# Optimization experiments

Hardware: AMD Instinct MI355X
Metric: run time of the kernel (lower is better)

The kernel has to match this reference:

```python
import jax, jax.numpy as jnp
import numpy as np

DIM = 256
NUM_EXPERTS = 16
EXPERT_HIDDEN = 128
ROUTER_HIDDEN = 64
N_TOKENS = 32768


def setup_inputs() -> dict:
    key = jax.random.key(0)
    ks = jax.random.split(key, 9)
    s = lambda fan_in: 1.0 / np.sqrt(fan_in)
    x = jax.random.normal(ks[0], (N_TOKENS, DIM), dtype=jnp.float32)
    # Router params (Linear(DIM,64) -> ReLU -> Linear(64,E))
    r_w1 = jax.random.uniform(ks[1], (DIM, ROUTER_HIDDEN), jnp.float32, -s(DIM), s(DIM))
    r_b1 = jax.random.uniform(ks[2], (ROUTER_HIDDEN,), jnp.float32, -s(DIM), s(DIM))
    r_w2 = jax.random.uniform(ks[3], (ROUTER_HIDDEN, NUM_EXPERTS), jnp.float32, -s(ROUTER_HIDDEN), s(ROUTER_HIDDEN))
    r_b2 = jax.random.uniform(ks[4], (NUM_EXPERTS,), jnp.float32, -s(ROUTER_HIDDEN), s(ROUTER_HIDDEN))
    # Expert params, stacked over experts: Linear(DIM,128) -> Tanh -> Linear(128,DIM)
    e_w1 = jax.random.uniform(ks[5], (NUM_EXPERTS, DIM, EXPERT_HIDDEN), jnp.float32, -s(DIM), s(DIM))
    e_b1 = jax.random.uniform(ks[6], (NUM_EXPERTS, EXPERT_HIDDEN), jnp.float32, -s(DIM), s(DIM))
    e_w2 = jax.random.uniform(ks[7], (NUM_EXPERTS, EXPERT_HIDDEN, DIM), jnp.float32, -s(EXPERT_HIDDEN), s(EXPERT_HIDDEN))
    e_b2 = jax.random.uniform(ks[8], (NUM_EXPERTS, DIM), jnp.float32, -s(EXPERT_HIDDEN), s(EXPERT_HIDDEN))
    return {"x": x, "r_w1": r_w1, "r_b1": r_b1, "r_w2": r_w2, "r_b2": r_b2,
            "e_w1": e_w1, "e_b1": e_b1, "e_w2": e_w2, "e_b2": e_b2}


def reference(x, r_w1, r_b1, r_w2, r_b2, e_w1, e_b1, e_w2, e_b2):
    # Router: softmax(Linear(ReLU(Linear(x)))), temp=1.0
    h_r = jax.nn.relu(x @ r_w1 + r_b1)                      # [N, 64]
    w = jax.nn.softmax(h_r @ r_w2 + r_b2, axis=-1)          # [N, E]
    # All experts densely (faithful to the reference loop), batched over E.
    h = jnp.tanh(jnp.einsum('nd,edh->neh', x, e_w1) + e_b1[None, :, :])   # [N, E, H]
    outs = jnp.einsum('neh,ehd->ned', h, e_w2) + e_b2[None, :, :]         # [N, E, D]
    # Top-2 gating: mask, renormalize, combine.
    top_val, top_idx = jax.lax.top_k(w, 2)                  # [N, 2]
    n = w.shape[0]
    mask = jnp.zeros_like(w).at[jnp.arange(n)[:, None], top_idx].set(1.0)
    w_top = w * mask
    w_top = w_top / (jnp.sum(w_top, axis=-1, keepdims=True) + 1e-8)
    y_pred = jnp.einsum('ne,ned->nd', w_top, outs)          # [N, D]
    return (y_pred, w)
```

## Files before the change

kernel.cpp:

```cpp
#include <hip/hip_runtime.h>
#include <math.h>

#define NT 32768
#define DIM 256
#define NE 16
#define EH 128
#define RH 64
#define TB 128

#define IB (NT * DIM)
#define WS_COUNTS (IB)
#define WS_OFFSETS (IB + 16)
#define WS_CURSORS (IB + 33)
#define WS_NBLK (IB + 49)
#define WS_TABLE (IB + 64)
#define WS_TOKE (IB + 4096)
#define WS_LIST (WS_TOKE + 2 * NT)
#define WS_TOKG (WS_LIST + 2 * NT)
#define WS_LIST_G (WS_TOKG + 2 * NT)
#define WS_END_I (WS_LIST_G + 2 * NT)
#define U_W1T (2 * WS_END_I)
#define U_W2T (U_W1T + NE * DIM * EH)

typedef __attribute__((ext_vector_type(4))) float f32x4;
typedef __attribute__((ext_vector_type(8))) short bf16x8;
typedef __attribute__((ext_vector_type(8))) unsigned short us8;

#define SWZ(b) ((b) ^ (((b) >> 4) & 0x70))

__device__ inline unsigned short f2bf(float f) {
    unsigned int bits = __builtin_bit_cast(unsigned int, f);
    bits += 0x7fffu + ((bits >> 16) & 1u);
    return (unsigned short)(bits >> 16);
}

__global__ __launch_bounds__(256) void router_kernel(
    const float* __restrict__ x,
    const float* __restrict__ rw1, const float* __restrict__ rb1,
    const float* __restrict__ rw2, const float* __restrict__ rb2,
    float* __restrict__ w_out, int* __restrict__ wsi, float* __restrict__ wsf)
{
    __shared__ float xT[64][68];
    __shared__ float w1s[64][64];
    __shared__ float hs[64][68];
    __shared__ float ls[64][20];
    __shared__ int scnt[16];

    const int tid = threadIdx.x;
    const int tok0 = blockIdx.x * 64;
    if (tid < 16) scnt[tid] = 0;

    float acc[4][4];
#pragma unroll
    for (int i = 0; i < 4; ++i)
#pragma unroll
        for (int j = 0; j < 4; ++j) acc[i][j] = 0.f;

    const int tt = (tid & 15) * 4;
    const int hh = (tid >> 4) * 4;

    for (int kc = 0; kc < 4; ++kc) {
        __syncthreads();
#pragma unroll
        for (int i = 0; i < 4; ++i) {
            int idx = tid + 256 * i;
            int t = idx >> 4;
            int d4 = (idx & 15) * 4;
            float4 v = *(const float4*)(x + (size_t)(tok0 + t) * DIM + kc * 64 + d4);
            xT[d4 + 0][t] = v.x; xT[d4 + 1][t] = v.y;
            xT[d4 + 2][t] = v.z; xT[d4 + 3][t] = v.w;
        }
#pragma unroll
        for (int i = 0; i < 4; ++i) {
            int idx = tid + 256 * i;
            int d = idx >> 4;
            int h4 = (idx & 15) * 4;
            *(float4*)&w1s[d][h4] = *(const float4*)(rw1 + (size_t)(kc * 64 + d) * RH + h4);
        }
        __syncthreads();
#pragma unroll 8
        for (int d = 0; d < 64; ++d) {
            const float4 xa4 = *(const float4*)&xT[d][tt];
            const float4 wv4 = *(const float4*)&w1s[d][hh];
            const float xa[4] = {xa4.x, xa4.y, xa4.z, xa4.w};
            const float wv[4] = {wv4.x, wv4.y, wv4.z, wv4.w};
#pragma unroll
            for (int i = 0; i < 4; ++i)
#pragma unroll
                for (int j = 0; j < 4; ++j)
                    acc[i][j] = fmaf(xa[i], wv[j], acc[i][j]);
        }
    }
    __syncthreads();
    {
        const float4 b4 = *(const float4*)(rb1 + hh);
        const float b[4] = {b4.x, b4.y, b4.z, b4.w};
#pragma unroll
        for (int i = 0; i < 4; ++i) {
            float4 hv;
            hv.x = fmaxf(acc[i][0] + b[0], 0.f);
            hv.y = fmaxf(acc[i][1] + b[1], 0.f);
            hv.z = fmaxf(acc[i][2] + b[2], 0.f);
            hv.w = fmaxf(acc[i][3] + b[3], 0.f);
            *(float4*)&hs[tt + i][hh] = hv;
        }
    }
    __syncthreads();
    {
        int tok = tid >> 2;
        int e0 = (tid & 3) * 4;
        float l[4] = {0.f, 0.f, 0.f, 0.f};
#pragma unroll 8
        for (int k = 0; k < 64; ++k) {
            float hv = hs[tok][k];
            float4 wv = *(const float4*)(rw2 + k * NE + e0);
            l[0] = fmaf(hv, wv.x, l[0]);
            l[1] = fmaf(hv, wv.y, l[1]);
            l[2] = fmaf(hv, wv.z, l[2]);
            l[3] = fmaf(hv, wv.w, l[3]);
        }
        float4 lb = *(const float4*)(rb2 + e0);
        ls[tok][e0 + 0] = l[0] + lb.x;
        ls[tok][e0 + 1] = l[1] + lb.y;
        ls[tok][e0 + 2] = l[2] + lb.z;
        ls[tok][e0 + 3] = l[3] + lb.w;
    }
    __syncthreads();
    if (tid < 64) {
        const int tok = tid;
        const int gt = tok0 + tok;
        float v[16];
        float m = -1e30f;
#pragma unroll
        for (int e = 0; e < 16; ++e) { v[e] = ls[tok][e]; m = fmaxf(m, v[e]); }
        float s = 0.f;
#pragma unroll
        for (int e = 0; e < 16; ++e) { v[e] = expf(v[e] - m); s += v[e]; }
        const float inv = 1.0f / s;
#pragma unroll
        for (int e = 0; e < 16; ++e) v[e] *= inv;
#pragma unroll
        for (int e = 0; e < 16; e += 4) {
            float4 wv = make_float4(v[e], v[e + 1], v[e + 2], v[e + 3]);
            *(float4*)(w_out + (size_t)gt * NE + e) = wv;
        }
        float v1 = -1.f, v2 = -1.f; int i1 = 0, i2 = 0;
#pragma unroll
        for (int e = 0; e < 16; ++e) {
            if (v[e] > v1) { v2 = v1; i2 = i1; v1 = v[e]; i1 = e; }
            else if (v[e] > v2) { v2 = v[e]; i2 = e; }
        }
        const float den = v1 + v2 + 1e-8f;
        atomicAdd(&scnt[i1], 1);
        atomicAdd(&scnt[i2], 1);
        wsi[WS_TOKE + 2 * gt + 0] = i1;
        wsi[WS_TOKE + 2 * gt + 1] = i2;
        wsf[WS_TOKG + 2 * gt + 0] = v1 / den;
        wsf[WS_TOKG + 2 * gt + 1] = v2 / den;
    }
    __syncthreads();
    if (tid < 16 && scnt[tid]) atomicAdd(&wsi[WS_COUNTS + tid], scnt[tid]);
}

__global__ __launch_bounds__(256) void wprep_kernel(
    const float* __restrict__ ew1, const float* __restrict__ ew2,
    unsigned short* __restrict__ w1t, unsigned short* __restrict__ w2t)
{
    __shared__ float t[64][65];
    int b = blockIdx.x;
    const float* src; unsigned short* dst; int R, C, tr, tc;
    if (b < 128) {
        int e = b >> 3, t8 = b & 7; tr = t8 >> 1; tc = t8 & 1;
        src = ew1 + (size_t)e * DIM * EH; R = DIM; C = EH;
        dst = w1t + (size_t)e * DIM * EH;
    } else {
        int b2 = b - 128; int e = b2 >> 3, t8 = b2 & 7; tr = t8 & 1; tc = t8 >> 1;
        src = ew2 + (size_t)e * EH * DIM; R = EH; C = DIM;
        dst = w2t + (size_t)e * EH * DIM;
    }
    const int R0 = tr * 64, C0 = tc * 64;
    const int tid = threadIdx.x;
#pragma unroll
    for (int q = 0; q < 4; ++q) {
        int r = (tid >> 4) + q * 16, c = (tid & 15) * 4;
        float4 v = *(const float4*)(src + (size_t)(R0 + r) * C + C0 + c);
        t[r][c] = v.x; t[r][c + 1] = v.y; t[r][c + 2] = v.z; t[r][c + 3] = v.w;
    }
    __syncthreads();
#pragma unroll
    for (int q = 0; q < 2; ++q) {
        int rp = (tid >> 3) + q * 32, c0 = (tid & 7) * 8;
        us8 u;
#pragma unroll
        for (int k = 0; k < 8; ++k) u[k] = f2bf(t[c0 + k][rp]);
        *(us8*)(dst + (size_t)(C0 + rp) * R + R0 + c0) = u;
    }
}

__global__ __launch_bounds__(64) void scan_kernel(int* __restrict__ wsi)
{
    __shared__ int soff[17], snc[16];
    const int tid = threadIdx.x;
    if (tid == 0) {
        int off = 0, nb = 0;
        soff[0] = 0;
        for (int e = 0; e < NE; ++e) {
            int c = wsi[WS_COUNTS + e];
            wsi[WS_CURSORS + e] = off;
            wsi[WS_OFFSETS + e] = off;
            off += c;
            soff[e + 1] = off;
            snc[e] = nb;
            nb += (c + TB - 1) / TB;
        }
        wsi[WS_OFFSETS + NE] = off;
        wsi[WS_NBLK] = nb;
    }
    __syncthreads();
    for (int e = 0; e < NE; ++e) {
        int nc = (soff[e + 1] - soff[e] + TB - 1) / TB;
        for (int k = tid; k < nc; k += 64)
            wsi[WS_TABLE + snc[e] + k] = (e << 16) | k;
    }
}

__global__ __launch_bounds__(256) void scatter_kernel(int* __restrict__ wsi, float* __restrict__ wsf)
{
    __shared__ int scnt[16], sbase[16];
    const int tid = threadIdx.x;
    const int t = blockIdx.x * 256 + tid;
    if (tid < 16) scnt[tid] = 0;
    __syncthreads();
    const int e0 = wsi[WS_TOKE + 2 * t + 0];
    const int e1 = wsi[WS_TOKE + 2 * t + 1];
    const int l0 = atomicAdd(&scnt[e0], 1);
    const int l1 = atomicAdd(&scnt[e1], 1);
    __syncthreads();
    if (tid < 16) sbase[tid] = scnt[tid] ? atomicAdd(&wsi[WS_CURSORS + tid], scnt[tid]) : 0;
    __syncthreads();
    const int p0 = sbase[e0] + l0;
    const int p1 = sbase[e1] + l1;
    wsi[WS_LIST + p0] = (t << 1);
    wsf[WS_LIST_G + p0] = wsf[WS_TOKG + 2 * t + 0];
    wsi[WS_LIST + p1] = (t << 1) | 1;
    wsf[WS_LIST_G + p1] = wsf[WS_TOKG + 2 * t + 1];
}

__global__ __launch_bounds__(256) void expert_kernel(
    const float* __restrict__ x,
    const float* __restrict__ eb1, const float* __restrict__ eb2,
    const unsigned short* __restrict__ w1t, const unsigned short* __restrict__ w2t,
    const int* __restrict__ wsi, const float* __restrict__ wsf,
    float* __restrict__ y, float* __restrict__ part1)
{
    __shared__ unsigned short smem[32768];
    if ((int)blockIdx.x >= wsi[WS_NBLK]) return;

    const int ent = wsi[WS_TABLE + blockIdx.x];
    const int e = ent >> 16;
    const int c = ent & 0xffff;
    const int start = wsi[WS_OFFSETS + e] + c * TB;
    const int cnt = min(TB, wsi[WS_OFFSETS + e + 1] - start);

    const int tid = threadIdx.x;
    const int lane = tid & 63, w = tid >> 6;
    const int wm = w >> 1, wn = w & 1;
    const int l15 = lane & 15;
    const int lk2 = ((lane >> 4) * 8) * 2;
    const int q4 = (lane >> 4) * 4;

    const int sr = tid >> 1, side = tid & 1;
    const int srow = (sr < cnt) ? (wsi[WS_LIST + start + sr] >> 1) : -1;

    char* lds = (char*)smem;

    f32x4 zero4; zero4[0] = zero4[1] = zero4[2] = zero4[3] = 0.f;
    f32x4 acc[4][4];
#pragma unroll
    for (int i = 0; i < 4; ++i)
#pragma unroll
        for (int j = 0; j < 4; ++j) acc[i][j] = zero4;

    for (int kh = 0; kh < 2; ++kh) {
        __syncthreads();
        {
            const int base = sr * 256 + side * 128;
            const float* xr = x + (size_t)(srow < 0 ? 0 : srow) * DIM + kh * 128 + side * 64;
#pragma unroll
            for (int i = 0; i < 8; ++i) {
                us8 u;
                if (srow >= 0) {
                    float4 a = *(const float4*)(xr + i * 8);
                    float4 b = *(const float4*)(xr + i * 8 + 4);
                    u[0] = f2bf(a.x); u[1] = f2bf(a.y); u[2] = f2bf(a.z); u[3] = f2bf(a.w);
                    u[4] = f2bf(b.x); u[5] = f2bf(b.y); u[6] = f2bf(b.z); u[7] = f2bf(b.w);
                } else {
#pragma unroll
                    for (int k = 0; k < 8; ++k) u[k] = 0;
                }
                *(us8*)(lds + SWZ(base + i * 16)) = u;
            }
        }
        {
            const unsigned short* wr = w1t + (size_t)e * DIM * EH + sr * 256 + kh * 128 + side * 64;
            const int base = 32768 + sr * 256 + side * 128;
#pragma unroll
            for (int i = 0; i < 8; ++i)
                *(us8*)(lds + SWZ(base + i * 16)) = *(const us8*)(wr + i * 8);
        }
        __syncthreads();
#pragma unroll
        for (int ks = 0; ks < 4; ++ks) {
            bf16x8 a[4], b[4];
#pragma unroll
            for (int mt = 0; mt < 4; ++mt) {
                int row = wm * 64 + mt * 16 + l15;
                a[mt] = *(const bf16x8*)(lds + SWZ(row * 256 + ks * 64 + lk2));
            }
#pragma unroll
            for (int nt = 0; nt < 4; ++nt) {
                int h = wn * 64 + nt * 16 + l15;
                b[nt] = *(const bf16x8*)(lds + SWZ(32768 + h * 256 + ks * 64 + lk2));
            }
#pragma unroll
            for (int mt = 0; mt < 4; ++mt)
#pragma unroll
                for (int nt = 0; nt < 4; ++nt)
                    acc[mt][nt] = __builtin_amdgcn_mfma_f32_16x16x32_bf16(a[mt], b[nt], acc[mt][nt], 0, 0, 0);
        }
    }

    __syncthreads();
#pragma unroll
    for (int nt = 0; nt < 4; ++nt) {
        const int col = wn * 64 + nt * 16 + l15;
        const float b1v = eb1[e * EH + col];
#pragma unroll
        for (int mt = 0; mt < 4; ++mt)
#pragma unroll
            for (int r = 0; r < 4; ++r) {
                int row = wm * 64 + mt * 16 + q4 + r;
                *(unsigned short*)(lds + SWZ(row * 256 + col * 2)) = f2bf(tanhf(acc[mt][nt][r] + b1v));
            }
    }
    {
        const unsigned short* wr = w2t + (size_t)e * EH * DIM + (size_t)sr * 128 + side * 64;
        const int base = 32768 + sr * 256 + side * 128;
#pragma unroll
        for (int i = 0; i < 8; ++i)
            *(us8*)(lds + SWZ(base + i * 16)) = *(const us8*)(wr + i * 8);
    }
    __syncthreads();

    for (int dh = 0; dh < 2; ++dh) {
        if (dh == 1) {
            __syncthreads();
            const unsigned short* wr = w2t + (size_t)e * EH * DIM + (size_t)(128 + sr) * 128 + side * 64;
            const int base = 32768 + sr * 256 + side * 128;
#pragma unroll
            for (int i = 0; i < 8; ++i)
                *(us8*)(lds + SWZ(base + i * 16)) = *(const us8*)(wr + i * 8);
            __syncthreads();
        }
        f32x4 acc2[4][4];
#pragma unroll
        for (int i = 0; i < 4; ++i)
#pragma unroll
            for (int j = 0; j < 4; ++j) acc2[i][j] = zero4;
#pragma unroll
        for (int ks = 0; ks < 4; ++ks) {
            bf16x8 a[4], b[4];
#pragma unroll
            for (int mt = 0; mt < 4; ++mt) {
                int row = wm * 64 + mt * 16 + l15;
                a[mt] = *(const bf16x8*)(lds + SWZ(row * 256 + ks * 64 + lk2));
            }
#pragma unroll
            for (int nt = 0; nt < 4; ++nt) {
                int d = wn * 64 + nt * 16 + l15;
                b[nt] = *(const bf16x8*)(lds + SWZ(32768 + d * 256 + ks * 64 + lk2));
            }
#pragma unroll
            for (int mt = 0; mt < 4; ++mt)
#pragma unroll
                for (int nt = 0; nt < 4; ++nt)
                    acc2[mt][nt] = __builtin_amdgcn_mfma_f32_16x16x32_bf16(a[mt], b[nt], acc2[mt][nt], 0, 0, 0);
        }
        float b2v[4];
#pragma unroll
        for (int nt = 0; nt < 4; ++nt)
            b2v[nt] = eb2[e * DIM + dh * 128 + wn * 64 + nt * 16 + l15];
#pragma unroll
        for (int mt = 0; mt < 4; ++mt)
#pragma unroll
            for (int r = 0; r < 4; ++r) {
                int rl = wm * 64 + mt * 16 + q4 + r;
                if (rl < cnt) {
                    int entry = wsi[WS_LIST + start + rl];
                    int tok = entry >> 1;
                    float g = wsf[WS_LIST_G + start + rl];
                    float* dst = ((entry & 1) ? part1 : y) + (size_t)tok * DIM + dh * 128 + wn * 64;
#pragma unroll
                    for (int nt = 0; nt < 4; ++nt)
                        dst[nt * 16 + l15] = g * (acc2[mt][nt][r] + b2v[nt]);
                }
            }
    }
}

__global__ __launch_bounds__(256) void combine_kernel(float* __restrict__ y,
                                                      const float* __restrict__ part1)
{
    const size_t i = ((size_t)blockIdx.x * 256 + threadIdx.x) * 4;
    float4 a = *(float4*)(y + i);
    const float4 b = *(const float4*)(part1 + i);
    a.x += b.x; a.y += b.y; a.z += b.z; a.w += b.w;
    *(float4*)(y + i) = a;
}

extern "C" void kernel_launch(void* const* d_in, const int* in_sizes, int n_in,
                              void* d_out, int out_size, void* d_ws, size_t ws_size,
                              hipStream_t stream)
{
    const float* x = (const float*)d_in[0];
    const float* rw1 = (const float*)d_in[1];
    const float* rb1 = (const float*)d_in[2];
    const float* rw2 = (const float*)d_in[3];
    const float* rb2 = (const float*)d_in[4];
    const float* ew1 = (const float*)d_in[5];
    const float* eb1 = (const float*)d_in[6];
    const float* ew2 = (const float*)d_in[7];
    const float* eb2 = (const float*)d_in[8];

    float* y = (float*)d_out;
    float* w_out = y + (size_t)NT * DIM;
    int* wsi = (int*)d_ws;
    float* wsf = (float*)d_ws;
    float* part1 = (float*)d_ws;
    unsigned short* wsu = (unsigned short*)d_ws;

    hipMemsetAsync(wsi + WS_COUNTS, 0, NE * sizeof(int), stream);

    wprep_kernel<<<256, 256, 0, stream>>>(ew1, ew2, wsu + U_W1T, wsu + U_W2T);
    router_kernel<<<NT / 64, 256, 0, stream>>>(x, rw1, rb1, rw2, rb2, w_out, wsi, wsf);
    scan_kernel<<<1, 64, 0, stream>>>(wsi);
    scatter_kernel<<<NT / 256, 256, 0, stream>>>(wsi, wsf);
    expert_kernel<<<2 * NT / TB + NE, 256, 0, stream>>>(x, eb1, eb2, wsu + U_W1T, wsu + U_W2T,
                                                        wsi, wsf, y, part1);
    combine_kernel<<<NT * DIM / 1024, 256, 0, stream>>>(y, part1);
}
```

Baseline: 129.6 us.

## Shrink expert tile to 64 tokens and read weights straight from global

Halves the token tile per block to 64 rows and stages only the activation tile in LDS (32 KB), with each wave reading its expert weight fragments directly from global/L2 instead of staging them in LDS. The goal is more resident blocks per CU (launch bounds 4), fewer barriers and better load balance across the per-expert chunks. The cost is less weight reuse per block: weights are fetched twice as often overall, and uncoalesced per-lane global reads now feed the MFMAs directly, which can stall them.

```diff
diff --git a/kernel.cpp b/kernel.cpp
--- a/kernel.cpp
+++ b/kernel.cpp
@@ -6,7 +6,7 @@
 #define NE 16
 #define EH 128
 #define RH 64
-#define TB 128
+#define TB 64
 
 #define IB (NT * DIM)
 #define WS_COUNTS (IB)
@@ -26,7 +26,8 @@
 typedef __attribute__((ext_vector_type(8))) short bf16x8;
 typedef __attribute__((ext_vector_type(8))) unsigned short us8;
 
-#define SWZ(b) ((b) ^ (((b) >> 4) & 0x70))
+#define SWZ9(b) ((b) ^ (((b) >> 5) & 0x70))
+#define SWZ8(b) ((b) ^ (((b) >> 4) & 0x70))
 
 __device__ inline unsigned short f2bf(float f) {
     unsigned int bits = __builtin_bit_cast(unsigned int, f);
@@ -246,14 +247,14 @@
     wsf[WS_LIST_G + p1] = wsf[WS_TOKG + 2 * t + 1];
 }
 
-__global__ __launch_bounds__(256) void expert_kernel(
+__global__ __launch_bounds__(256, 4) void expert_kernel(
     const float* __restrict__ x,
     const float* __restrict__ eb1, const float* __restrict__ eb2,
     const unsigned short* __restrict__ w1t, const unsigned short* __restrict__ w2t,
     const int* __restrict__ wsi, const float* __restrict__ wsf,
     float* __restrict__ y, float* __restrict__ part1)
 {
-    __shared__ unsigned short smem[32768];
+    __shared__ unsigned short smem[16384];
     if ((int)blockIdx.x >= wsi[WS_NBLK]) return;
 
     const int ent = wsi[WS_TABLE + blockIdx.x];
@@ -264,144 +265,115 @@
 
     const int tid = threadIdx.x;
     const int lane = tid & 63, w = tid >> 6;
-    const int wm = w >> 1, wn = w & 1;
     const int l15 = lane & 15;
-    const int lk2 = ((lane >> 4) * 8) * 2;
-    const int q4 = (lane >> 4) * 4;
-
-    const int sr = tid >> 1, side = tid & 1;
-    const int srow = (sr < cnt) ? (wsi[WS_LIST + start + sr] >> 1) : -1;
-
+    const int kq = lane >> 4;
+    const int q4 = kq * 4;
     char* lds = (char*)smem;
 
+    {
+        const int row = tid >> 2, q = tid & 3;
+        const int srow = (row < cnt) ? (wsi[WS_LIST + start + row] >> 1) : -1;
+        const float* xr = x + (size_t)(srow < 0 ? 0 : srow) * DIM + q * 64;
+        const int base = row * 512 + q * 128;
+#pragma unroll
+        for (int i = 0; i < 8; ++i) {
+            us8 u;
+            if (srow >= 0) {
+                float4 a = *(const float4*)(xr + i * 8);
+                float4 b = *(const float4*)(xr + i * 8 + 4);
+                u[0] = f2bf(a.x); u[1] = f2bf(a.y); u[2] = f2bf(a.z); u[3] = f2bf(a.w);
+                u[4] = f2bf(b.x); u[5] = f2bf(b.y); u[6] = f2bf(b.z); u[7] = f2bf(b.w);
+            } else {
+#pragma unroll
+                for (int k = 0; k < 8; ++k) u[k] = 0;
+            }
+            *(us8*)(lds + SWZ9(base + i * 16)) = u;
+        }
+    }
+    __syncthreads();
+
     f32x4 zero4; zero4[0] = zero4[1] = zero4[2] = zero4[3] = 0.f;
-    f32x4 acc[4][4];
+    f32x4 acc[4][2];
 #pragma unroll
     for (int i = 0; i < 4; ++i)
 #pragma unroll
-        for (int j = 0; j < 4; ++j) acc[i][j] = zero4;
-
-    for (int kh = 0; kh < 2; ++kh) {
-        __syncthreads();
-        {
-            const int base = sr * 256 + side * 128;
-            const float* xr = x + (size_t)(srow < 0 ? 0 : srow) * DIM + kh * 128 + side * 64;
-#pragma unroll
-            for (int i = 0; i < 8; ++i) {
-                us8 u;
-                if (srow >= 0) {
-                    float4 a = *(const float4*)(xr + i * 8);
-                    float4 b = *(const float4*)(xr + i * 8 + 4);
-                    u[0] = f2bf(a.x); u[1] = f2bf(a.y); u[2] = f2bf(a.z); u[3] = f2bf(a.w);
-                    u[4] = f2bf(b.x); u[5] = f2bf(b.y); u[6] = f2bf(b.z); u[7] = f2bf(b.w);
-                } else {
-#pragma unroll
-                    for (int k = 0; k < 8; ++k) u[k] = 0;
-                }
-                *(us8*)(lds + SWZ(base + i * 16)) = u;
+        for (int j = 0; j < 2; ++j) acc[i][j] = zero4;
+
+    const char* w1e = (const char*)(w1t + (size_t)e * DIM * EH);
+#pragma unroll
+    for (int ks = 0; ks < 8; ++ks) {
+        bf16x8 a[4], b[2];
+#pragma unroll
+        for (int nt = 0; nt < 2; ++nt) {
+            int h = w * 32 + nt * 16 + l15;
+            b[nt] = *(const bf16x8*)(w1e + h * 512 + ks * 64 + kq * 16);
+        }
+#pragma unroll
+        for (int mt = 0; mt < 4; ++mt)
+            a[mt] = *(const bf16x8*)(lds + SWZ9((mt * 16 + l15) * 512 + ks * 64 + kq * 16));
+#pragma unroll
+        for (int mt = 0; mt < 4; ++mt)
+#pragma unroll
+            for (int nt = 0; nt < 2; ++nt)
+                acc[mt][nt] = __builtin_amdgcn_mfma_f32_16x16x32_bf16(a[mt], b[nt], acc[mt][nt], 0, 0, 0);
+    }
+    __syncthreads();
+
+#pragma unroll
+    for (int nt = 0; nt < 2; ++nt) {
+        const int h = w * 32 + nt * 16 + l15;
+        const float b1v = eb1[e * EH + h];
+#pragma unroll
+        for (int mt = 0; mt < 4; ++mt)
+#pragma unroll
+            for (int r = 0; r < 4; ++r) {
+                int tok = mt * 16 + q4 + r;
+                *(unsigned short*)(lds + SWZ8(tok * 256 + h * 2)) = f2bf(tanhf(acc[mt][nt][r] + b1v));
             }
-        }
-        {
-            const unsigned short* wr = w1t + (size_t)e * DIM * EH + sr * 256 + kh * 128 + side * 64;
-            const int base = 32768 + sr * 256 + side * 128;
-#pragma unroll
-            for (int i = 0; i < 8; ++i)
-                *(us8*)(lds + SWZ(base + i * 16)) = *(const us8*)(wr + i * 8);
-        }
-        __syncthreads();
+    }
+    __syncthreads();
+
+    const char* w2e = (const char*)(w2t + (size_t)e * EH * DIM);
+#pragma unroll
+    for (int half = 0; half < 2; ++half) {
+        f32x4 acc2[4][2];
+#pragma unroll
+        for (int i = 0; i < 4; ++i)
+#pragma unroll
+            for (int j = 0; j < 2; ++j) acc2[i][j] = zero4;
 #pragma unroll
         for (int ks = 0; ks < 4; ++ks) {
-            bf16x8 a[4], b[4];
-#pragma unroll
-            for (int mt = 0; mt < 4; ++mt) {
-                int row = wm * 64 + mt * 16 + l15;
-                a[mt] = *(const bf16x8*)(lds + SWZ(row * 256 + ks * 64 + lk2));
+            bf16x8 a[4], b[2];
+#pragma unroll
+            for (int nt = 0; nt < 2; ++nt) {
+                int d = w * 64 + half * 32 + nt * 16 + l15;
+                b[nt] = *(const bf16x8*)(w2e + d * 256 + ks * 64 + kq * 16);
             }
 #pragma unroll
-            for (int nt = 0; nt < 4; ++nt) {
-                int h = wn * 64 + nt * 16 + l15;
-                b[nt] = *(const bf16x8*)(lds + SWZ(32768 + h * 256 + ks * 64 + lk2));
-            }
-#pragma unroll
             for (int mt = 0; mt < 4; ++mt)
-#pragma unroll
-                for (int nt = 0; nt < 4; ++nt)
-                    acc[mt][nt] = __builtin_amdgcn_mfma_f32_16x16x32_bf16(a[mt], b[nt], acc[mt][nt], 0, 0, 0);
-        }
-    }
-
-    __syncthreads();
-#pragma unroll
-    for (int nt = 0; nt < 4; ++nt) {
-        const int col = wn * 64 + nt * 16 + l15;
-        const float b1v = eb1[e * EH + col];
+                a[mt] = *(const bf16x8*)(lds + SWZ8((mt * 16 + l15) * 256 + ks * 64 + kq * 16));
+#pragma unroll
+            for (int mt = 0; mt < 4; ++mt)
+#pragma unroll
+                for (int nt = 0; nt < 2; ++nt)
+                    acc2[mt][nt] = __builtin_amdgcn_mfma_f32_16x16x32_bf16(a[mt], b[nt], acc2[mt][nt], 0, 0, 0);
+        }
+        float b2v[2];
+#pragma unroll
+        for (int nt = 0; nt < 2; ++nt)
+            b2v[nt] = eb2[e * DIM + w * 64 + half * 32 + nt * 16 + l15];
 #pragma unroll
         for (int mt = 0; mt < 4; ++mt)
 #pragma unroll
             for (int r = 0; r < 4; ++r) {
-                int row = wm * 64 + mt * 16 + q4 + r;
-                *(unsigned short*)(lds + SWZ(row * 256 + col * 2)) = f2bf(tanhf(acc[mt][nt][r] + b1v));
-            }
-    }
-    {
-        const unsigned short* wr = w2t + (size_t)e * EH * DIM + (size_t)sr * 128 + side * 64;
-        const int base = 32768 + sr * 256 + side * 128;
-#pragma unroll
-        for (int i = 0; i < 8; ++i)
-            *(us8*)(lds + SWZ(base + i * 16)) = *(const us8*)(wr + i * 8);
-    }
-    __syncthreads();
-
-    for (int dh = 0; dh < 2; ++dh) {
-        if (dh == 1) {
-            __syncthreads();
-            const unsigned short* wr = w2t + (size_t)e * EH * DIM + (size_t)(128 + sr) * 128 + side * 64;
-            const int base = 32768 + sr * 256 + side * 128;
-#pragma unroll
-            for (int i = 0; i < 8; ++i)
-                *(us8*)(lds + SWZ(base + i * 16)) = *(const us8*)(wr + i * 8);
-            __syncthreads();
-        }
-        f32x4 acc2[4][4];
-#pragma unroll
-        for (int i = 0; i < 4; ++i)
-#pragma unroll
-            for (int j = 0; j < 4; ++j) acc2[i][j] = zero4;
-#pragma unroll
-        for (int ks = 0; ks < 4; ++ks) {
-            bf16x8 a[4], b[4];
-#pragma unroll
-            for (int mt = 0; mt < 4; ++mt) {
-                int row = wm * 64 + mt * 16 + l15;
-                a[mt] = *(const bf16x8*)(lds + SWZ(row * 256 + ks * 64 + lk2));
-            }
-#pragma unroll
-            for (int nt = 0; nt < 4; ++nt) {
-                int d = wn * 64 + nt * 16 + l15;
-                b[nt] = *(const bf16x8*)(lds + SWZ(32768 + d * 256 + ks * 64 + lk2));
-            }
-#pragma unroll
-            for (int mt = 0; mt < 4; ++mt)
-#pragma unroll
-                for (int nt = 0; nt < 4; ++nt)
-                    acc2[mt][nt] = __builtin_amdgcn_mfma_f32_16x16x32_bf16(a[mt], b[nt], acc2[mt][nt], 0, 0, 0);
-        }
-        float b2v[4];
-#pragma unroll
-        for (int nt = 0; nt < 4; ++nt)
-            b2v[nt] = eb2[e * DIM + dh * 128 + wn * 64 + nt * 16 + l15];
-#pragma unroll
-        for (int mt = 0; mt < 4; ++mt)
-#pragma unroll
-            for (int r = 0; r < 4; ++r) {
-                int rl = wm * 64 + mt * 16 + q4 + r;
+                int rl = mt * 16 + q4 + r;
                 if (rl < cnt) {
                     int entry = wsi[WS_LIST + start + rl];
                     int tok = entry >> 1;
                     float g = wsf[WS_LIST_G + start + rl];
-                    float* dst = ((entry & 1) ? part1 : y) + (size_t)tok * DIM + dh * 128 + wn * 64;
-#pragma unroll
-                    for (int nt = 0; nt < 4; ++nt)
+                    float* dst = ((entry & 1) ? part1 : y) + (size_t)tok * DIM + w * 64 + half * 32;
+#pragma unroll
+                    for (int nt = 0; nt < 2; ++nt)
                         dst[nt * 16 + l15] = g * (acc2[mt][nt][r] + b2v[nt]);
                 }
             }
```

After: 133.3 us. +2.8%, slower.
